# Kernel optimization log

Hardware: AMD Instinct MI355X
Metric: run time of the kernel (lower is better)

Reference implementation:

```python
import jax, jax.numpy as jnp
import numpy as np

HIDDEN = 256
HORIZON = 24
FMET = 16
OUT = 1
EPS = 1e-5


def setup_inputs() -> dict:
    key = jax.random.key(0)
    ks = jax.random.split(key, 12)
    B, N = 16, 1000
    final_h = jax.random.normal(ks[0], (B, N, HIDDEN), dtype=jnp.float32)
    future_met = jax.random.normal(ks[1], (B, HORIZON, N, FMET), dtype=jnp.float32)
    # step_queries: xavier_uniform over (max_horizon, hidden)
    lim_q = float(np.sqrt(6.0 / (HORIZON + HIDDEN)))
    step_queries = jax.random.uniform(ks[2], (HORIZON, HIDDEN), minval=-lim_q, maxval=lim_q, dtype=jnp.float32)
    # future_met_proj: Linear(FMET -> HIDDEN); store weight as (FMET, HIDDEN)
    lim_fm = float(np.sqrt(1.0 / FMET))
    W_fm = jax.random.uniform(ks[3], (FMET, HIDDEN), minval=-lim_fm, maxval=lim_fm, dtype=jnp.float32)
    b_fm = jax.random.uniform(ks[4], (HIDDEN,), minval=-lim_fm, maxval=lim_fm, dtype=jnp.float32)
    gamma = jnp.ones((HIDDEN,), dtype=jnp.float32)
    beta = jnp.zeros((HIDDEN,), dtype=jnp.float32)
    lim1 = float(np.sqrt(1.0 / HIDDEN))
    W1 = jax.random.uniform(ks[5], (HIDDEN, HIDDEN), minval=-lim1, maxval=lim1, dtype=jnp.float32)
    b1 = jax.random.uniform(ks[6], (HIDDEN,), minval=-lim1, maxval=lim1, dtype=jnp.float32)
    W2 = jax.random.uniform(ks[7], (HIDDEN, OUT), minval=-lim1, maxval=lim1, dtype=jnp.float32)
    b2 = jax.random.uniform(ks[8], (OUT,), minval=-lim1, maxval=lim1, dtype=jnp.float32)
    return {
        "final_h": final_h,
        "future_met": future_met,
        "step_queries": step_queries,
        "W_fm": W_fm,
        "b_fm": b_fm,
        "gamma": gamma,
        "beta": beta,
        "W1": W1,
        "b1": b1,
        "W2": W2,
        "b2": b2,
    }


def _layer_norm(x, gamma, beta):
    mu = jnp.mean(x, axis=-1, keepdims=True)
    var = jnp.mean(jnp.square(x - mu), axis=-1, keepdims=True)
    return (x - mu) * jax.lax.rsqrt(var + EPS) * gamma + beta


def reference(final_h, future_met, step_queries, W_fm, b_fm, gamma, beta, W1, b1, W2, b2):
    # final_h: (B, N, H); future_met: (B, T, N, F)
    # combined: (B, N, T, H) = broadcast(final_h) + queries + proj(future_met)
    combined = final_h[:, :, None, :] + step_queries[None, None, :, :]
    fm = jnp.transpose(future_met, (0, 2, 1, 3))  # (B, N, T, F)
    combined = combined + (jnp.einsum("bntf,fh->bnth", fm, W_fm) + b_fm)
    x = _layer_norm(combined, gamma, beta)
    x = jax.nn.gelu(x @ W1 + b1, approximate=False)
    # dropout is identity in eval mode
    out = x @ W2 + b2  # (B, N, T, OUT)
    return jnp.transpose(out, (0, 2, 1, 3))  # (B, T, N, OUT)
```

## Files before the change

### kernel.cpp

```cpp
#include <hip/hip_runtime.h>
#include <hip/hip_bf16.h>
#include <stdint.h>

#define MROWS 32
#define LDA   264
#define FMS   40

typedef __bf16 bf16x8 __attribute__((ext_vector_type(8)));
typedef float  f32x4  __attribute__((ext_vector_type(4)));

__device__ __forceinline__ unsigned short f2bf(float f) {
    union { float f; uint32_t u; } v; v.f = f;
    return (unsigned short)((v.u + 0x7FFFu + ((v.u >> 16) & 1u)) >> 16);
}

__device__ __forceinline__ ushort2 pk_bf16(float a, float b) {
    union { __hip_bfloat162 v; ushort2 u; } c;
    c.v = __float22bfloat162_rn(make_float2(a, b));
    return c.u;
}

__device__ __forceinline__ float gelu_fast(float v) {
    const float t = v * v;
    const float p = fmaf(0.044715f, t, 1.0f);
    const float u = v * p;
    const float e = __builtin_amdgcn_exp2f(u * -2.3021131160186336f);
    return v * __builtin_amdgcn_rcpf(1.0f + e);
}

__device__ __forceinline__ int frag_n(int f) {
    return (f & 0xC0) | ((f & 3) << 4) | ((f >> 2) & 15);
}

__global__ __launch_bounds__(256) void prep1(const float* __restrict__ W1,
                                             const float* __restrict__ step_q,
                                             const float* __restrict__ b_fm,
                                             const float* __restrict__ W_fm,
                                             const float* __restrict__ gamma,
                                             const float* __restrict__ beta,
                                             unsigned short* __restrict__ w1frag,
                                             float* __restrict__ sqb,
                                             unsigned short* __restrict__ wfmfrag,
                                             float* __restrict__ gpart,
                                             float* __restrict__ bpart) {
    const int blk = blockIdx.x, tid = threadIdx.x;
    if (blk < 8) {
        __shared__ unsigned short T[256][40];
        const int kk = blk;
        float sg = 0.f, sb = 0.f;
        #pragma unroll
        for (int r = 0; r < 32; ++r) {
            const int k = (kk << 5) + r;
            const float wv = W1[k * 256 + tid];
            sg = fmaf(gamma[k], wv, sg);
            sb = fmaf(beta[k],  wv, sb);
            T[tid][r] = f2bf(wv);
        }
        gpart[(kk << 8) + tid] = sg;
        bpart[(kk << 8) + tid] = sb;
        __syncthreads();
        #pragma unroll
        for (int f = 0; f < 4; ++f) {
            const int fi = (f << 8) + tid;
            const int l = fi & 63, j = (fi >> 6) & 3, w = fi >> 8;
            const int n = (w << 6) + (j << 4) + (l & 15);
            const uint4 v = *(const uint4*)&T[n][(l >> 4) << 3];
            *(uint4*)&w1frag[((w << 5) + (j << 3) + kk) * 512 + (l << 3)] = v;
        }
    } else if (blk < 32) {
        const int t = blk - 8;
        const int n = frag_n(tid);
        sqb[t * 256 + tid] = step_q[t * 256 + n] + b_fm[n];
    } else {
        const int f  = blk - 32;
        const int fr = (f << 8) + tid;
        const int l = fr & 63, j = (fr >> 6) & 3, w = fr >> 8;
        const int n = (w << 6) + (j << 4) + (l & 15);
        const int qr = l >> 4;
        #pragma unroll
        for (int e = 0; e < 8; ++e) {
            const int k = (qr << 3) + e;
            wfmfrag[(fr << 3) + e] = (k < 16) ? f2bf(W_fm[(k << 8) + n]) : (unsigned short)0;
        }
    }
}

__global__ __launch_bounds__(256) void prep2(const float* __restrict__ gpart,
                                             const float* __restrict__ bpart,
                                             const float* __restrict__ b1,
                                             const float* __restrict__ W2,
                                             const float* __restrict__ gamma,
                                             float* __restrict__ gw1f,
                                             float* __restrict__ b1tf,
                                             float* __restrict__ w2f,
                                             float* __restrict__ gamf) {
    const int tid = threadIdx.x;
    const int n = frag_n(tid);
    float sg = 0.f, sb = 0.f;
    #pragma unroll
    for (int kk = 0; kk < 8; ++kk) {
        sg += gpart[(kk << 8) + n];
        sb += bpart[(kk << 8) + n];
    }
    gw1f[tid] = sg;
    b1tf[tid] = sb + b1[n];
    w2f[tid]  = W2[n];
    gamf[tid] = gamma[n];
}

__global__ __launch_bounds__(256, 6) void fused_head(
    const float* __restrict__ final_h, const float* __restrict__ future_met,
    const float* __restrict__ b2,      const unsigned short* __restrict__ w1frag,
    const float* __restrict__ sqb,     const unsigned short* __restrict__ wfmfrag,
    const float* __restrict__ gw1f,    const float* __restrict__ b1tf,
    const float* __restrict__ w2f,     const float* __restrict__ gamf,
    float* __restrict__ out)
{
    __shared__ __align__(16) unsigned short Abuf[MROWS * LDA];
    __shared__ __align__(16) unsigned short fmA[MROWS * FMS];
    __shared__ float2 red[4][MROWS];
    __shared__ float2 mv[MROWS];
    __shared__ float  part[4][MROWS];

    const int tid = threadIdx.x;
    const int w   = tid >> 6;
    const int l   = tid & 63;
    const int col = l & 15;
    const int qr  = l >> 4;
    const int m0  = blockIdx.x * MROWS;
    const int bn0 = m0 / 24;
    const int tt0 = m0 - bn0 * 24;
    const int fb  = (w << 6) + (col << 2);

    if (tid < 128) {
        const int row = tid >> 2, f0 = (tid & 3) << 2;
        const int tta = tt0 + row;
        const int sub = (tta >= 24) + (tta >= 48);
        const int tt  = tta - sub * 24;
        const int bn  = bn0 + sub;
        const int b   = bn / 1000, n = bn - b * 1000;
        const float4 v = *(const float4*)&future_met[((((b * 24 + tt) * 1000) + n) << 4) + f0];
        ushort2 lo = pk_bf16(v.x, v.y), hi = pk_bf16(v.z, v.w);
        ushort4 o; o.x = lo.x; o.y = lo.y; o.z = hi.x; o.w = hi.y;
        *(ushort4*)&fmA[row * FMS + f0] = o;
    }
    {
        const int row = tid >> 3, k = 16 + ((tid & 7) << 1);
        *(unsigned int*)&fmA[row * FMS + k] = 0u;
    }
    __syncthreads();

    const float4 g4 = *(const float4*)&gamf[fb];
    const float g_[4] = {g4.x, g4.y, g4.z, g4.w};

    f32x4 acc[2][4];
    #pragma unroll
    for (int i = 0; i < 2; ++i) {
        #pragma unroll
        for (int r = 0; r < 4; ++r) {
            const int d   = (i << 4) + (qr << 2) + r;
            const int tta = tt0 + d;
            const int sub = (tta >= 24) + (tta >= 48);
            const int tt  = tta - sub * 24;
            const int bn  = bn0 + sub;
            const float* fh = final_h + (bn << 8) + (w << 6) + col;
            const float4 sb4 = *(const float4*)&sqb[(tt << 8) + fb];
            acc[i][0][r] = fh[0]  + sb4.x;
            acc[i][1][r] = fh[16] + sb4.y;
            acc[i][2][r] = fh[32] + sb4.z;
            acc[i][3][r] = fh[48] + sb4.w;
        }
    }
    {
        const bf16x8 af0 = *(const bf16x8*)&fmA[col * FMS + (qr << 3)];
        const bf16x8 af1 = *(const bf16x8*)&fmA[(16 + col) * FMS + (qr << 3)];
        const unsigned short* Bwf = wfmfrag + (w << 11) + (l << 3);
        #pragma unroll
        for (int j = 0; j < 4; ++j) {
            const bf16x8 bf = *(const bf16x8*)(Bwf + (j << 9));
            acc[0][j] = __builtin_amdgcn_mfma_f32_16x16x32_bf16(af0, bf, acc[0][j], 0, 0, 0);
            acc[1][j] = __builtin_amdgcn_mfma_f32_16x16x32_bf16(af1, bf, acc[1][j], 0, 0, 0);
        }
    }

    #pragma unroll
    for (int i = 0; i < 2; ++i) {
        #pragma unroll
        for (int r = 0; r < 4; ++r) {
            const int m = (i << 4) + (qr << 2) + r;
            float s = 0.f, q = 0.f, vj[4];
            #pragma unroll
            for (int j = 0; j < 4; ++j) {
                const float v = acc[i][j][r];
                s += v; q = fmaf(v, v, q);
                vj[j] = v * g_[j];
            }
            s += __shfl_xor(s, 1); q += __shfl_xor(q, 1);
            s += __shfl_xor(s, 2); q += __shfl_xor(q, 2);
            s += __shfl_xor(s, 4); q += __shfl_xor(q, 4);
            s += __shfl_xor(s, 8); q += __shfl_xor(q, 8);
            if (col == 0) red[w][m] = make_float2(s, q);
            const ushort2 p01 = pk_bf16(vj[0], vj[1]);
            const ushort2 p23 = pk_bf16(vj[2], vj[3]);
            unsigned short* Ab = &Abuf[m * LDA + (w << 6) + col];
            Ab[0]  = p01.x; Ab[16] = p01.y;
            Ab[32] = p23.x; Ab[48] = p23.y;
        }
    }
    __syncthreads();

    if (tid < MROWS) {
        const float2 a0 = red[0][tid], a1 = red[1][tid], a2 = red[2][tid], a3 = red[3][tid];
        const float S = a0.x + a1.x + a2.x + a3.x;
        const float Q = a0.y + a1.y + a2.y + a3.y;
        const float mu = S * 0.00390625f;
        const float rstd = rsqrtf(Q * 0.00390625f - mu * mu + 1e-5f);
        mv[tid] = make_float2(mu, rstd);
    }

    #pragma unroll
    for (int i = 0; i < 2; ++i)
        #pragma unroll
        for (int j = 0; j < 4; ++j)
            acc[i][j] = (f32x4){0.f, 0.f, 0.f, 0.f};

    {
        const unsigned short* Bw  = w1frag + (w << 14) + (l << 3);
        const unsigned short* Ab0 = &Abuf[col * LDA + (qr << 3)];
        const unsigned short* Ab1 = &Abuf[(16 + col) * LDA + (qr << 3)];
        #pragma unroll
        for (int kk = 0; kk < 8; ++kk) {
            const bf16x8 a0 = *(const bf16x8*)(Ab0 + (kk << 5));
            const bf16x8 a1 = *(const bf16x8*)(Ab1 + (kk << 5));
            #pragma unroll
            for (int j = 0; j < 4; ++j) {
                const bf16x8 bf = *(const bf16x8*)(Bw + (j << 12) + (kk << 9));
                acc[0][j] = __builtin_amdgcn_mfma_f32_16x16x32_bf16(a0, bf, acc[0][j], 0, 0, 0);
                acc[1][j] = __builtin_amdgcn_mfma_f32_16x16x32_bf16(a1, bf, acc[1][j], 0, 0, 0);
            }
        }
    }

    const float4 gw4 = *(const float4*)&gw1f[fb];
    const float4 bt4 = *(const float4*)&b1tf[fb];
    const float4 w24 = *(const float4*)&w2f[fb];
    const float gwv[4] = {gw4.x, gw4.y, gw4.z, gw4.w};
    const float btv[4] = {bt4.x, bt4.y, bt4.z, bt4.w};
    const float w2v[4] = {w24.x, w24.y, w24.z, w24.w};
    __syncthreads();

    #pragma unroll
    for (int i = 0; i < 2; ++i) {
        #pragma unroll
        for (int r = 0; r < 4; ++r) {
            const int m = (i << 4) + (qr << 2) + r;
            const float2 p = mv[m];
            const float cm = -p.x * p.y;
            float pp = 0.f;
            #pragma unroll
            for (int j = 0; j < 4; ++j) {
                const float yv = fmaf(p.y, acc[i][j][r], fmaf(cm, gwv[j], btv[j]));
                const float g = gelu_fast(yv);
                pp = fmaf(g, w2v[j], pp);
            }
            pp += __shfl_xor(pp, 1);
            pp += __shfl_xor(pp, 2);
            pp += __shfl_xor(pp, 4);
            pp += __shfl_xor(pp, 8);
            if (col == 0) part[w][m] = pp;
        }
    }
    __syncthreads();

    if (tid < MROWS) {
        const int m = m0 + tid;
        const float val = part[0][tid] + part[1][tid] + part[2][tid] + part[3][tid] + b2[0];
        const int bn = m / 24, tt = m - bn * 24;
        const int b  = bn / 1000, n = bn - b * 1000;
        out[(b * 24 + tt) * 1000 + n] = val;
    }
}

extern "C" void kernel_launch(void* const* d_in, const int* in_sizes, int n_in,
                              void* d_out, int out_size, void* d_ws, size_t ws_size,
                              hipStream_t stream) {
    const float* final_h    = (const float*)d_in[0];
    const float* future_met = (const float*)d_in[1];
    const float* step_q     = (const float*)d_in[2];
    const float* W_fm       = (const float*)d_in[3];
    const float* b_fm       = (const float*)d_in[4];
    const float* gamma      = (const float*)d_in[5];
    const float* beta       = (const float*)d_in[6];
    const float* W1         = (const float*)d_in[7];
    const float* b1         = (const float*)d_in[8];
    const float* W2         = (const float*)d_in[9];
    const float* b2         = (const float*)d_in[10];

    unsigned short* w1frag  = (unsigned short*)d_ws;
    float*          sqb     = (float*)((char*)d_ws + 131072);
    unsigned short* wfmfrag = (unsigned short*)((char*)d_ws + 155648);
    float*          gpart   = (float*)((char*)d_ws + 188416);
    float*          bpart   = (float*)((char*)d_ws + 196608);
    float*          gw1f    = (float*)((char*)d_ws + 204800);
    float*          b1tf    = (float*)((char*)d_ws + 205824);
    float*          w2f     = (float*)((char*)d_ws + 206848);
    float*          gamf    = (float*)((char*)d_ws + 207872);
    float* out = (float*)d_out;

    prep1<<<36, 256, 0, stream>>>(W1, step_q, b_fm, W_fm, gamma, beta,
                                  w1frag, sqb, wfmfrag, gpart, bpart);
    prep2<<<1, 256, 0, stream>>>(gpart, bpart, b1, W2, gamma, gw1f, b1tf, w2f, gamf);
    fused_head<<<12000, 256, 0, stream>>>(final_h, future_met, b2,
                                          w1frag, sqb, wfmfrag, gw1f, b1tf, w2f, gamf, out);
}
```

Before: 225.0 us.

## Compute LayerNorm statistics via MFMA and fold gamma into W1 fragments

Folds gamma into the bf16 W1 weights during prep, so the main kernel stores raw pre-norm activations to LDS without a per-element gamma multiply. Row sums and sums of squares are computed with extra MFMA instructions (A times a ones vector, and A times itself) inside the GEMM loop. This replaces the shuffle reduction, the shared-memory reduction and one barrier. Statistics now come from bf16-rounded values, which may cost some accuracy, and launch bounds drop from 6 to 5 blocks per CU to leave room for the extra accumulators.

```diff
diff --git a/kernel.cpp b/kernel.cpp
--- a/kernel.cpp
+++ b/kernel.cpp
@@ -52,9 +52,10 @@
         for (int r = 0; r < 32; ++r) {
             const int k = (kk << 5) + r;
             const float wv = W1[k * 256 + tid];
-            sg = fmaf(gamma[k], wv, sg);
-            sb = fmaf(beta[k],  wv, sb);
-            T[tid][r] = f2bf(wv);
+            const float gk = gamma[k];
+            sg = fmaf(gk, wv, sg);
+            sb = fmaf(beta[k], wv, sb);
+            T[tid][r] = f2bf(gk * wv);
         }
         gpart[(kk << 8) + tid] = sg;
         bpart[(kk << 8) + tid] = sb;
@@ -89,11 +90,9 @@
                                              const float* __restrict__ bpart,
                                              const float* __restrict__ b1,
                                              const float* __restrict__ W2,
-                                             const float* __restrict__ gamma,
                                              float* __restrict__ gw1f,
                                              float* __restrict__ b1tf,
-                                             float* __restrict__ w2f,
-                                             float* __restrict__ gamf) {
+                                             float* __restrict__ w2f) {
     const int tid = threadIdx.x;
     const int n = frag_n(tid);
     float sg = 0.f, sb = 0.f;
@@ -105,21 +104,17 @@
     gw1f[tid] = sg;
     b1tf[tid] = sb + b1[n];
     w2f[tid]  = W2[n];
-    gamf[tid] = gamma[n];
-}
-
-__global__ __launch_bounds__(256, 6) void fused_head(
+}
+
+__global__ __launch_bounds__(256, 5) void fused_head(
     const float* __restrict__ final_h, const float* __restrict__ future_met,
     const float* __restrict__ b2,      const unsigned short* __restrict__ w1frag,
     const float* __restrict__ sqb,     const unsigned short* __restrict__ wfmfrag,
     const float* __restrict__ gw1f,    const float* __restrict__ b1tf,
-    const float* __restrict__ w2f,     const float* __restrict__ gamf,
-    float* __restrict__ out)
+    const float* __restrict__ w2f,     float* __restrict__ out)
 {
     __shared__ __align__(16) unsigned short Abuf[MROWS * LDA];
     __shared__ __align__(16) unsigned short fmA[MROWS * FMS];
-    __shared__ float2 red[4][MROWS];
-    __shared__ float2 mv[MROWS];
     __shared__ float  part[4][MROWS];
 
     const int tid = threadIdx.x;
@@ -149,9 +144,6 @@
         *(unsigned int*)&fmA[row * FMS + k] = 0u;
     }
     __syncthreads();
-
-    const float4 g4 = *(const float4*)&gamf[fb];
-    const float g_[4] = {g4.x, g4.y, g4.z, g4.w};
 
     f32x4 acc[2][4];
     #pragma unroll
@@ -188,20 +180,8 @@
         #pragma unroll
         for (int r = 0; r < 4; ++r) {
             const int m = (i << 4) + (qr << 2) + r;
-            float s = 0.f, q = 0.f, vj[4];
-            #pragma unroll
-            for (int j = 0; j < 4; ++j) {
-                const float v = acc[i][j][r];
-                s += v; q = fmaf(v, v, q);
-                vj[j] = v * g_[j];
-            }
-            s += __shfl_xor(s, 1); q += __shfl_xor(q, 1);
-            s += __shfl_xor(s, 2); q += __shfl_xor(q, 2);
-            s += __shfl_xor(s, 4); q += __shfl_xor(q, 4);
-            s += __shfl_xor(s, 8); q += __shfl_xor(q, 8);
-            if (col == 0) red[w][m] = make_float2(s, q);
-            const ushort2 p01 = pk_bf16(vj[0], vj[1]);
-            const ushort2 p23 = pk_bf16(vj[2], vj[3]);
+            const ushort2 p01 = pk_bf16(acc[i][0][r], acc[i][1][r]);
+            const ushort2 p23 = pk_bf16(acc[i][2][r], acc[i][3][r]);
             unsigned short* Ab = &Abuf[m * LDA + (w << 6) + col];
             Ab[0]  = p01.x; Ab[16] = p01.y;
             Ab[32] = p23.x; Ab[48] = p23.y;
@@ -209,20 +189,16 @@
     }
     __syncthreads();
 
-    if (tid < MROWS) {
-        const float2 a0 = red[0][tid], a1 = red[1][tid], a2 = red[2][tid], a3 = red[3][tid];
-        const float S = a0.x + a1.x + a2.x + a3.x;
-        const float Q = a0.y + a1.y + a2.y + a3.y;
-        const float mu = S * 0.00390625f;
-        const float rstd = rsqrtf(Q * 0.00390625f - mu * mu + 1e-5f);
-        mv[tid] = make_float2(mu, rstd);
-    }
-
     #pragma unroll
     for (int i = 0; i < 2; ++i)
         #pragma unroll
         for (int j = 0; j < 4; ++j)
             acc[i][j] = (f32x4){0.f, 0.f, 0.f, 0.f};
+    f32x4 accS[2] = {(f32x4){0.f,0.f,0.f,0.f}, (f32x4){0.f,0.f,0.f,0.f}};
+    f32x4 accQ[2] = {(f32x4){0.f,0.f,0.f,0.f}, (f32x4){0.f,0.f,0.f,0.f}};
+    bf16x8 ones;
+    #pragma unroll
+    for (int e = 0; e < 8; ++e) ones[e] = (__bf16)1.0f;
 
     {
         const unsigned short* Bw  = w1frag + (w << 14) + (l << 3);
@@ -232,6 +208,10 @@
         for (int kk = 0; kk < 8; ++kk) {
             const bf16x8 a0 = *(const bf16x8*)(Ab0 + (kk << 5));
             const bf16x8 a1 = *(const bf16x8*)(Ab1 + (kk << 5));
+            accS[0] = __builtin_amdgcn_mfma_f32_16x16x32_bf16(a0, ones, accS[0], 0, 0, 0);
+            accS[1] = __builtin_amdgcn_mfma_f32_16x16x32_bf16(a1, ones, accS[1], 0, 0, 0);
+            accQ[0] = __builtin_amdgcn_mfma_f32_16x16x32_bf16(a0, a0, accQ[0], 0, 0, 0);
+            accQ[1] = __builtin_amdgcn_mfma_f32_16x16x32_bf16(a1, a1, accQ[1], 0, 0, 0);
             #pragma unroll
             for (int j = 0; j < 4; ++j) {
                 const bf16x8 bf = *(const bf16x8*)(Bw + (j << 12) + (kk << 9));
@@ -247,19 +227,21 @@
     const float gwv[4] = {gw4.x, gw4.y, gw4.z, gw4.w};
     const float btv[4] = {bt4.x, bt4.y, bt4.z, bt4.w};
     const float w2v[4] = {w24.x, w24.y, w24.z, w24.w};
-    __syncthreads();
-
+
+    const int sbase = (qr << 4) + (qr << 2);
     #pragma unroll
     for (int i = 0; i < 2; ++i) {
         #pragma unroll
         for (int r = 0; r < 4; ++r) {
             const int m = (i << 4) + (qr << 2) + r;
-            const float2 p = mv[m];
-            const float cm = -p.x * p.y;
+            const float mu = accS[i][r] * 0.00390625f;
+            const float qv = __shfl(accQ[i][r], sbase + r);
+            const float rstd = rsqrtf(fmaf(-mu, mu, qv * 0.00390625f) + 1e-5f);
+            const float cm = -mu * rstd;
             float pp = 0.f;
             #pragma unroll
             for (int j = 0; j < 4; ++j) {
-                const float yv = fmaf(p.y, acc[i][j][r], fmaf(cm, gwv[j], btv[j]));
+                const float yv = fmaf(rstd, acc[i][j][r], fmaf(cm, gwv[j], btv[j]));
                 const float g = gelu_fast(yv);
                 pp = fmaf(g, w2v[j], pp);
             }
@@ -304,12 +286,11 @@
     float*          gw1f    = (float*)((char*)d_ws + 204800);
     float*          b1tf    = (float*)((char*)d_ws + 205824);
     float*          w2f     = (float*)((char*)d_ws + 206848);
-    float*          gamf    = (float*)((char*)d_ws + 207872);
     float* out = (float*)d_out;
 
     prep1<<<36, 256, 0, stream>>>(W1, step_q, b_fm, W_fm, gamma, beta,
                                   w1frag, sqb, wfmfrag, gpart, bpart);
-    prep2<<<1, 256, 0, stream>>>(gpart, bpart, b1, W2, gamma, gw1f, b1tf, w2f, gamf);
+    prep2<<<1, 256, 0, stream>>>(gpart, bpart, b1, W2, gw1f, b1tf, w2f);
     fused_head<<<12000, 256, 0, stream>>>(final_h, future_met, b2,
-                                          w1frag, sqb, wfmfrag, gw1f, b1tf, w2f, gamf, out);
-}
+                                          w1frag, sqb, wfmfrag, gw1f, b1tf, w2f, out);
+}
```

New measurement: 238.5 us. 6.0% more time.
